# Performance work log

Hardware: AMD Instinct MI355X
Metric: run time of the kernel (lower is better)

## Reference

```python
import jax, jax.numpy as jnp
import numpy as np

BATCH = 2_000_000
N = 8
ALPHA = 0.002
MAX_NUM_ITER = 100


def _build_A():
    # Circulant second-difference operator scaled by n^2 (periodic Laplacian)
    a = np.eye(N) * 2 - np.eye(N, k=1) - np.eye(N, k=-1)
    a[-1, 0] = -1.0
    a[0, -1] = -1.0
    a *= N ** 2
    return jnp.asarray(a, dtype=jnp.float32)


def setup_inputs() -> dict:
    key = jax.random.key(0)
    k1, k2 = jax.random.split(key)
    x = jax.random.normal(k1, (BATCH, N), dtype=jnp.float32)
    y = jax.random.normal(k2, (BATCH, N), dtype=jnp.float32)
    return {"x": x, "y": y, "A": _build_A()}


def reference(x, y, A):
    # x <- x + alpha * (y - x @ A), repeated max_num_iter times (strict sequential dep)
    def body(xc, _):
        r = y - xc @ A          # [B, 8] residual
        return xc + ALPHA * r, None

    x_final, _ = jax.lax.scan(body, x, None, length=MAX_NUM_ITER)
    return x_final
```

## Files before the change

kernel.cpp:

```cpp
#include <hip/hip_runtime.h>

#define ALPHA 0.002
#define NBLK 2048
#define BLK  256

typedef float fx4 __attribute__((ext_vector_type(4)));

__global__ __launch_bounds__(64) void build_PQ(const float* __restrict__ A,
                                               float* __restrict__ PQ) {
    const int tid = threadIdx.x;
    const int i = tid >> 3, j = tid & 7;
    __shared__ double Ms[64];
    __shared__ double Ps[64];
    __shared__ double Ss[64];

    const double m = ((i == j) ? 1.0 : 0.0) - (double)ALPHA * (double)A[tid];
    Ms[tid] = m;
    __syncthreads();

    double Mcol[8];
#pragma unroll
    for (int t = 0; t < 8; ++t) Mcol[t] = Ms[t * 8 + j];

    double P = (i == j) ? 1.0 : 0.0;
    double S = 0.0;
    const int bits[7] = {1, 1, 0, 0, 1, 0, 0};

#pragma unroll
    for (int b = 0; b < 7; ++b) {
        Ps[tid] = P;
        Ss[tid] = S;
        __syncthreads();
        double accS = S, accP = 0.0;
#pragma unroll
        for (int t = 0; t < 8; ++t) {
            const double pit = Ps[i * 8 + t];
            accS += pit * Ss[t * 8 + j];
            accP += pit * Ps[t * 8 + j];
        }
        __syncthreads();
        if (bits[b]) {
            S = accS + accP;
            Ps[tid] = accP;
            __syncthreads();
            double p2 = 0.0;
#pragma unroll
            for (int t = 0; t < 8; ++t) p2 += Ps[i * 8 + t] * Mcol[t];
            P = p2;
            __syncthreads();
        } else {
            S = accS;
            P = accP;
        }
    }

    PQ[tid]      = (float)P;
    PQ[64 + tid] = (float)((double)ALPHA * S);
}

__global__ __launch_bounds__(BLK) void apply_PQ(const fx4* __restrict__ x4,
                                                const fx4* __restrict__ y4,
                                                const float* __restrict__ PQ,
                                                fx4* __restrict__ out4,
                                                int nrows) {
    __shared__ float sP[64];
    __shared__ float sQ[64];
    if (threadIdx.x < 64) {
        sP[threadIdx.x] = PQ[threadIdx.x];
        sQ[threadIdx.x] = PQ[64 + threadIdx.x];
    }
    __syncthreads();

    const int stride = NBLK * BLK;
    int row = blockIdx.x * BLK + threadIdx.x;
    if (row >= nrows) return;

    size_t p = (size_t)row * 2;
    fx4 cx0 = x4[p], cx1 = x4[p + 1];
    fx4 cy0 = y4[p], cy1 = y4[p + 1];

    for (;;) {
        const int nrow = row + stride;
        const bool more = (nrow < nrows);
        fx4 nx0, nx1, ny0, ny1;
        if (more) {
            const size_t np = (size_t)nrow * 2;
            nx0 = x4[np]; nx1 = x4[np + 1];
            ny0 = y4[np]; ny1 = y4[np + 1];
        }

        const float xs[8] = {cx0.x, cx0.y, cx0.z, cx0.w,
                             cx1.x, cx1.y, cx1.z, cx1.w};
        const float ys[8] = {cy0.x, cy0.y, cy0.z, cy0.w,
                             cy1.x, cy1.y, cy1.z, cy1.w};
        float ov[8];
#pragma unroll
        for (int jj = 0; jj < 8; ++jj) {
            float acc = 0.0f;
#pragma unroll
            for (int t = 0; t < 8; ++t) acc = fmaf(xs[t], sP[t * 8 + jj], acc);
#pragma unroll
            for (int t = 0; t < 8; ++t) acc = fmaf(ys[t], sQ[t * 8 + jj], acc);
            ov[jj] = acc;
        }
        fx4 o0 = {ov[0], ov[1], ov[2], ov[3]};
        fx4 o1 = {ov[4], ov[5], ov[6], ov[7]};
        out4[p]     = o0;
        out4[p + 1] = o1;

        if (!more) break;
        row = nrow;
        p = (size_t)row * 2;
        cx0 = nx0; cx1 = nx1; cy0 = ny0; cy1 = ny1;
    }
}

extern "C" void kernel_launch(void* const* d_in, const int* in_sizes, int n_in,
                              void* d_out, int out_size, void* d_ws, size_t ws_size,
                              hipStream_t stream) {
    const float* x = (const float*)d_in[0];
    const float* y = (const float*)d_in[1];
    const float* A = (const float*)d_in[2];
    float* out = (float*)d_out;
    float* PQ  = (float*)d_ws;

    const int nrows = in_sizes[0] / 8;

    build_PQ<<<1, 64, 0, stream>>>(A, PQ);

    apply_PQ<<<NBLK, BLK, 0, stream>>>((const fx4*)x, (const fx4*)y, PQ,
                                       (fx4*)out, nrows);
}
```

Measured before the change: 38.31 us.

## Fuse P/Q matrix construction into the apply kernel, computing it per block

Removes the separate single-block build kernel and its workspace round-trip. Each block now recomputes the 8x8 P and Q matrices in double precision in shared memory, while the first row loads of x and y are already issued and in flight. This drops one kernel launch and the serial dependency between the two kernels. In exchange every block repeats the small double-precision matrix-power computation with several barriers, and the row-bounds early return before the first load is gone.

Measured after the change: 37.20 us. 2.9% less time.

```diff
diff --git a/kernel.cpp b/kernel.cpp
--- a/kernel.cpp
+++ b/kernel.cpp
@@ -6,21 +6,35 @@
 
 typedef float fx4 __attribute__((ext_vector_type(4)));
 
-__global__ __launch_bounds__(64) void build_PQ(const float* __restrict__ A,
-                                               float* __restrict__ PQ) {
-    const int tid = threadIdx.x;
-    const int i = tid >> 3, j = tid & 7;
+__global__ __launch_bounds__(BLK) void fused_apply(const fx4* __restrict__ x4,
+                                                   const fx4* __restrict__ y4,
+                                                   const float* __restrict__ A,
+                                                   fx4* __restrict__ out4,
+                                                   int nrows) {
     __shared__ double Ms[64];
     __shared__ double Ps[64];
     __shared__ double Ss[64];
+    __shared__ float sP[64];
+    __shared__ float sQ[64];
 
-    const double m = ((i == j) ? 1.0 : 0.0) - (double)ALPHA * (double)A[tid];
-    Ms[tid] = m;
+    const int tid = threadIdx.x;
+    const int stride = NBLK * BLK;
+
+    int row = blockIdx.x * BLK + tid;
+    size_t p = (size_t)row * 2;
+    fx4 cx0 = x4[p], cx1 = x4[p + 1];
+    fx4 cy0 = y4[p], cy1 = y4[p + 1];
+
+    const int i = tid >> 3, j = tid & 7;
+    if (tid < 64)
+        Ms[tid] = ((i == j) ? 1.0 : 0.0) - (double)ALPHA * (double)A[tid];
     __syncthreads();
 
     double Mcol[8];
+    if (tid < 64) {
 #pragma unroll
-    for (int t = 0; t < 8; ++t) Mcol[t] = Ms[t * 8 + j];
+        for (int t = 0; t < 8; ++t) Mcol[t] = Ms[t * 8 + j];
+    }
 
     double P = (i == j) ? 1.0 : 0.0;
     double S = 0.0;
@@ -28,25 +42,27 @@
 
 #pragma unroll
     for (int b = 0; b < 7; ++b) {
-        Ps[tid] = P;
-        Ss[tid] = S;
+        if (tid < 64) { Ps[tid] = P; Ss[tid] = S; }
         __syncthreads();
         double accS = S, accP = 0.0;
+        if (tid < 64) {
 #pragma unroll
-        for (int t = 0; t < 8; ++t) {
-            const double pit = Ps[i * 8 + t];
-            accS += pit * Ss[t * 8 + j];
-            accP += pit * Ps[t * 8 + j];
+            for (int t = 0; t < 8; ++t) {
+                const double pit = Ps[i * 8 + t];
+                accS += pit * Ss[t * 8 + j];
+                accP += pit * Ps[t * 8 + j];
+            }
         }
         __syncthreads();
         if (bits[b]) {
-            S = accS + accP;
-            Ps[tid] = accP;
+            if (tid < 64) { S = accS + accP; Ps[tid] = accP; }
             __syncthreads();
-            double p2 = 0.0;
+            if (tid < 64) {
+                double p2 = 0.0;
 #pragma unroll
-            for (int t = 0; t < 8; ++t) p2 += Ps[i * 8 + t] * Mcol[t];
-            P = p2;
+                for (int t = 0; t < 8; ++t) p2 += Ps[i * 8 + t] * Mcol[t];
+                P = p2;
+            }
             __syncthreads();
         } else {
             S = accS;
@@ -54,30 +70,11 @@
         }
     }
 
-    PQ[tid]      = (float)P;
-    PQ[64 + tid] = (float)((double)ALPHA * S);
-}
-
-__global__ __launch_bounds__(BLK) void apply_PQ(const fx4* __restrict__ x4,
-                                                const fx4* __restrict__ y4,
-                                                const float* __restrict__ PQ,
-                                                fx4* __restrict__ out4,
-                                                int nrows) {
-    __shared__ float sP[64];
-    __shared__ float sQ[64];
-    if (threadIdx.x < 64) {
-        sP[threadIdx.x] = PQ[threadIdx.x];
-        sQ[threadIdx.x] = PQ[64 + threadIdx.x];
+    if (tid < 64) {
+        sP[tid] = (float)P;
+        sQ[tid] = (float)((double)ALPHA * S);
     }
     __syncthreads();
-
-    const int stride = NBLK * BLK;
-    int row = blockIdx.x * BLK + threadIdx.x;
-    if (row >= nrows) return;
-
-    size_t p = (size_t)row * 2;
-    fx4 cx0 = x4[p], cx1 = x4[p + 1];
-    fx4 cy0 = y4[p], cy1 = y4[p + 1];
 
     for (;;) {
         const int nrow = row + stride;
@@ -122,12 +119,9 @@
     const float* y = (const float*)d_in[1];
     const float* A = (const float*)d_in[2];
     float* out = (float*)d_out;
-    float* PQ  = (float*)d_ws;
 
     const int nrows = in_sizes[0] / 8;
 
-    build_PQ<<<1, 64, 0, stream>>>(A, PQ);
-
-    apply_PQ<<<NBLK, BLK, 0, stream>>>((const fx4*)x, (const fx4*)y, PQ,
-                                       (fx4*)out, nrows);
+    fused_apply<<<NBLK, BLK, 0, stream>>>((const fx4*)x, (const fx4*)y, A,
+                                          (fx4*)out, nrows);
 }
```
